# Optimization experiments

Hardware: AMD Instinct MI355X
Metric: run time of the kernel (lower is better)

The kernel has to match this reference:

```python
import jax, jax.numpy as jnp
import numpy as np
from jax import lax

DIM = 1024
INTER = 512
N_EXPERTS = 16
TOPK = 4
ROUTE_SCALE = 2.5
VOCAB = 32000


def setup_inputs() -> dict:
    key = jax.random.key(0)
    ks = jax.random.split(key, 8)
    x = jax.random.normal(ks[0], (2, 512, DIM), dtype=jnp.float32)
    input_ids = jax.random.randint(ks[1], (2, 512), 0, VOCAB)
    s = 0.02
    gate_w = jax.random.normal(ks[2], (N_EXPERTS, DIM), dtype=jnp.float32) * s
    gate_b = jax.random.normal(ks[3], (N_EXPERTS,), dtype=jnp.float32) * s
    # routed experts: w13 maps dim -> 2*inter (gate|up), w2 maps inter -> dim
    w13 = jax.random.normal(ks[4], (N_EXPERTS, 2 * INTER, DIM), dtype=jnp.float32) * s
    w2 = jax.random.normal(ks[5], (N_EXPERTS, DIM, INTER), dtype=jnp.float32) * s
    # shared expert
    w13_s = jax.random.normal(ks[6], (2 * INTER, DIM), dtype=jnp.float32) * s
    w2_s = jax.random.normal(ks[7], (DIM, INTER), dtype=jnp.float32) * s
    return {"x": x, "input_ids": input_ids, "gate_w": gate_w, "gate_b": gate_b,
            "w13": w13, "w2": w2, "w13_s": w13_s, "w2_s": w2_s}


def _silu_and_mul(gu):
    gate, up = jnp.split(gu, 2, axis=-1)
    return jax.nn.silu(gate) * up


def reference(x, input_ids, gate_w, gate_b, w13, w2, w13_s, w2_s):
    B, S, D = x.shape
    xt = x.reshape(-1, D)                      # [T, D]
    T = xt.shape[0]
    # ---- Gate (sigmoid score func, bias added for selection only) ----
    scores = jax.nn.sigmoid(xt.astype(jnp.float32) @ gate_w.T)   # [T, E]
    biased = scores + gate_b
    _, idx = lax.top_k(biased, TOPK)                             # [T, K] int
    w = jnp.take_along_axis(scores, idx, axis=-1)                # [T, K]
    w = w / jnp.sum(w, axis=-1, keepdims=True)                   # normalize (non-softmax)
    w = w * ROUTE_SCALE
    # ---- dispatch/combine as dense per-expert combine weights ----
    comb = jnp.zeros((T, N_EXPERTS), jnp.float32)
    comb = comb.at[jnp.arange(T)[:, None], idx].add(w)           # [T, E]
    comb = comb.astype(x.dtype)

    def expert_body(y, args):
        w13_e, w2_e, c_e = args                                  # [2I,D], [D,I], [T]
        h = _silu_and_mul(xt @ w13_e.T)                          # [T, I]
        return y + c_e[:, None] * (h @ w2_e.T), None

    y, _ = lax.scan(expert_body, jnp.zeros_like(xt), (w13, w2, comb.T))
    # ---- shared expert ----
    y = y + _silu_and_mul(xt @ w13_s.T) @ w2_s.T
    return y.astype(x.dtype).reshape(B, S, D)
```

## Files before the change

kernel.cpp:

```cpp
#include <hip/hip_runtime.h>
#include <hip/hip_bf16.h>
#include <math.h>

#define NTOK   1024
#define DIMX   1024
#define INTERX 512
#define NEXP   16
#define RSCALE 2.5f

typedef _Float16 f16x8 __attribute__((ext_vector_type(8)));
typedef _Float16 f16x4v __attribute__((ext_vector_type(4)));
typedef float    f32x4 __attribute__((ext_vector_type(4)));

#define N_W13  (NEXP * 2 * INTERX * DIMX)
#define N_W2   (NEXP * DIMX * INTERX)
#define N_W13S (2 * INTERX * DIMX)
#define N_W2S  (DIMX * INTERX)
#define N_X    (NTOK * DIMX)
#define N_CVT  ((size_t)N_W13 + N_W2 + N_W13S + N_W2S + N_X)

#define WS_COUNTS  0
#define WS_TOKIDX  256
#define WS_SLOTS   (WS_TOKIDX + NEXP * NTOK * 4)
#define WS_WQ      (WS_SLOTS + NTOK * 16)
#define WS_SEL     (WS_WQ + NTOK * 16)
#define WS_NT      (WS_SEL + NTOK * 16)
#define WS_TE      (WS_NT + 64)
#define WS_TM      (WS_TE + 1024)
#define WS_TR      (WS_TM + 1024)
#define WS_H       (WS_TR + 1024)
#define WS_YC      (WS_H + (size_t)5120 * 512 * 2)
#define WS_F16     (WS_YC + (size_t)5120 * 1024 * 4)
#define WS_NEED    (WS_F16 + N_CVT * 2)

#define SWZ(r, k) ((r) * 64 + ((k) ^ (((r) & 7) << 3)))

#define CVT_BLOCKS 3392

__device__ __forceinline__ f16x8 ldcvt(const float* __restrict__ p) {
    const float4 a = *(const float4*)p;
    const float4 b = *(const float4*)(p + 4);
    return (f16x8){(_Float16)a.x, (_Float16)a.y, (_Float16)a.z, (_Float16)a.w,
                   (_Float16)b.x, (_Float16)b.y, (_Float16)b.z, (_Float16)b.w};
}

__device__ __forceinline__ void gl_lds16(const _Float16* g, _Float16* l) {
    __builtin_amdgcn_global_load_lds(
        (const __attribute__((address_space(1))) void*)g,
        (__attribute__((address_space(3))) void*)l, 16, 0, 0);
}

__global__ __launch_bounds__(256) void cvt_all(
    const float* __restrict__ w13, const float* __restrict__ w2,
    const float* __restrict__ w13s, const float* __restrict__ w2s,
    const float* __restrict__ x, _Float16* __restrict__ dh)
{
    const size_t base8 = (size_t)blockIdx.x * 256 + threadIdx.x;
    float4 ra[4], rb[4];
#pragma unroll
    for (int it = 0; it < 4; ++it) {
        size_t off = (base8 + (size_t)it * (CVT_BLOCKS * 256)) * 8;
        const float* s;
        if (off < N_W13)                       s = w13 + off;
        else if ((off -= N_W13) < N_W2)        s = w2 + off;
        else if ((off -= N_W2) < N_W13S)       s = w13s + off;
        else if ((off -= N_W13S) < N_W2S)      s = w2s + off;
        else                                   s = x + (off - N_W2S);
        ra[it] = *(const float4*)s;
        rb[it] = *(const float4*)(s + 4);
    }
#pragma unroll
    for (int it = 0; it < 4; ++it) {
        const size_t i8 = base8 + (size_t)it * (CVT_BLOCKS * 256);
        f16x8 v = {(_Float16)ra[it].x, (_Float16)ra[it].y,
                   (_Float16)ra[it].z, (_Float16)ra[it].w,
                   (_Float16)rb[it].x, (_Float16)rb[it].y,
                   (_Float16)rb[it].z, (_Float16)rb[it].w};
        *(f16x8*)(dh + i8 * 8) = v;
    }
}

__global__ __launch_bounds__(256) void gate(
    const float* __restrict__ x, const float* __restrict__ gw,
    const float* __restrict__ gb,
    int* __restrict__ sel, float* __restrict__ wq)
{
    const int t    = blockIdx.x * 4 + (threadIdx.x >> 6);
    const int lane = threadIdx.x & 63;
    const int e    = lane & 15;
    const int q    = lane >> 4;

    const float4* xq = (const float4*)(x + (size_t)t * DIMX) + q * 64;
    const float4* gq = (const float4*)(gw + (size_t)e * DIMX) + q * 64;
    float s0 = 0.f, s1 = 0.f, s2 = 0.f, s3 = 0.f;
#pragma unroll 8
    for (int i = 0; i < 64; i += 2) {
        const float4 a = xq[i],     b = gq[i];
        const float4 c = xq[i + 1], d = gq[i + 1];
        s0 = fmaf(a.x, b.x, s0); s1 = fmaf(a.y, b.y, s1);
        s2 = fmaf(a.z, b.z, s2); s3 = fmaf(a.w, b.w, s3);
        s0 = fmaf(c.x, d.x, s0); s1 = fmaf(c.y, d.y, s1);
        s2 = fmaf(c.z, d.z, s2); s3 = fmaf(c.w, d.w, s3);
    }
    float acc = (s0 + s1) + (s2 + s3);
    acc += __shfl_xor(acc, 16);
    acc += __shfl_xor(acc, 32);

    const float sv = 1.f / (1.f + __expf(-acc));
    float v = (lane < 16) ? (sv + gb[e]) : -1e30f;

    float wk0, wk1, wk2, wk3; int ek0, ek1, ek2, ek3;
    float wsum = 0.f;
#pragma unroll
    for (int k = 0; k < 4; ++k) {
        float bestv = v; int besti = lane;
#pragma unroll
        for (int off = 8; off >= 1; off >>= 1) {
            const float ov = __shfl_xor(bestv, off);
            const int   oi = __shfl_xor(besti, off);
            if (ov > bestv || (ov == bestv && oi < besti)) { bestv = ov; besti = oi; }
        }
        besti = __shfl(besti, 0);
        const float sbest = __shfl(sv, besti);
        if (k == 0) { wk0 = sbest; ek0 = besti; }
        if (k == 1) { wk1 = sbest; ek1 = besti; }
        if (k == 2) { wk2 = sbest; ek2 = besti; }
        if (k == 3) { wk3 = sbest; ek3 = besti; }
        wsum += sbest;
        if (lane == besti) v = -1e30f;
    }
    const float scale = RSCALE / wsum;

    if (lane == 0) {
        sel[t * 4 + 0] = ek0;  wq[t * 4 + 0] = wk0 * scale;
        sel[t * 4 + 1] = ek1;  wq[t * 4 + 1] = wk1 * scale;
        sel[t * 4 + 2] = ek2;  wq[t * 4 + 2] = wk2 * scale;
        sel[t * 4 + 3] = ek3;  wq[t * 4 + 3] = wk3 * scale;
    }
}

__global__ __launch_bounds__(1024) void build(
    const int* __restrict__ sel,
    int* __restrict__ counts, int* __restrict__ tok_idx,
    int* __restrict__ slots,
    int* __restrict__ n_tiles, int* __restrict__ tile_e,
    int* __restrict__ tile_m0, int* __restrict__ tile_r0)
{
    __shared__ int lc[NEXP];
    const int t = threadIdx.x;
    if (t < NEXP) lc[t] = 0;
    __syncthreads();

    int e0 = sel[t * 4 + 0], e1 = sel[t * 4 + 1];
    int e2 = sel[t * 4 + 2], e3 = sel[t * 4 + 3];
    int p0 = atomicAdd(&lc[e0], 1);
    int p1 = atomicAdd(&lc[e1], 1);
    int p2 = atomicAdd(&lc[e2], 1);
    int p3 = atomicAdd(&lc[e3], 1);
    tok_idx[e0 * NTOK + p0] = t;  slots[t * 4 + 0] = (e0 << 10) | p0;
    tok_idx[e1 * NTOK + p1] = t;  slots[t * 4 + 1] = (e1 << 10) | p1;
    tok_idx[e2 * NTOK + p2] = t;  slots[t * 4 + 2] = (e2 << 10) | p2;
    tok_idx[e3 * NTOK + p3] = t;  slots[t * 4 + 3] = (e3 << 10) | p3;

    __syncthreads();
    if (t < NEXP) counts[t] = lc[t];
    if (t == 0) {
        int nt = 0, row = 0;
        for (int e = 0; e <= NEXP; ++e) {
            const int c = (e == NEXP) ? NTOK : lc[e];
            for (int m0 = 0; m0 < c; m0 += 128) {
                tile_e[nt]  = e;
                tile_m0[nt] = m0;
                tile_r0[nt] = row + m0;
                ++nt;
            }
            row += c;
        }
        n_tiles[0] = nt;
    }
}

#define WAITV8()  do { asm volatile("s_waitcnt vmcnt(8)" ::: "memory"); \
                       __builtin_amdgcn_sched_barrier(0); } while (0)
#define WAITV0()  do { asm volatile("s_waitcnt vmcnt(0)" ::: "memory"); \
                       __builtin_amdgcn_sched_barrier(0); } while (0)
#define RBAR()    do { __builtin_amdgcn_s_barrier(); \
                       __builtin_amdgcn_sched_barrier(0); } while (0)

__global__ __launch_bounds__(256, 2) void ffn1g(
    const _Float16* __restrict__ xh,
    const _Float16* __restrict__ w13h, const _Float16* __restrict__ w13sh,
    const int* __restrict__ counts, const int* __restrict__ tok_idx,
    const int* __restrict__ n_tiles, const int* __restrict__ tile_e,
    const int* __restrict__ tile_m0, const int* __restrict__ tile_r0,
    _Float16* __restrict__ h)
{
    const int tile = blockIdx.x >> 3;
    if (tile >= n_tiles[0]) return;
    const int y  = blockIdx.x & 7;
    const int e  = tile_e[tile];
    const int m0 = tile_m0[tile];
    const int rowbase = tile_r0[tile] - m0;
    const int Me = (e == NEXP) ? NTOK : counts[e];
    const int g0 = y * 64;

    const int tid = threadIdx.x, lane = tid & 63;
    const int wid = tid >> 6;
    const int wm = wid >> 1, wn = wid & 1;
    const int li = lane & 15, rk = (lane >> 4) * 8;

    const _Float16* Wh = (e == NEXP) ? w13sh : (w13h + (size_t)e * (2 * INTERX) * DIMX);

    __shared__ _Float16 T[2][256 * 64];

    const int lrow = lane >> 3;
    const int lc   = (lane & 7) ^ lrow;
    const _Float16* src[8];
    int ldsoff[8];
#pragma unroll
    for (int j = 0; j < 8; ++j) {
        const int c = wid * 8 + j;
        const int r = c * 8 + lrow;
        ldsoff[j] = c * 512;
        if (r < 128) {
            int ma = m0 + r; if (ma >= Me) ma = Me - 1;
            const int tok = (e == NEXP) ? ma : tok_idx[e * NTOK + ma];
            src[j] = xh + (size_t)tok * DIMX + lc * 8;
        } else {
            const int rb = r - 128;
            const int bwn = rb >> 6, bf = (rb >> 4) & 3, bli = rb & 15;
            const int wrow = ((bf & 2) ? INTERX : 0) + g0 + bwn * 32 + (bf & 1) * 16 + bli;
            src[j] = Wh + (size_t)wrow * DIMX + lc * 8;
        }
    }

    f32x4 acc[4][4];
#pragma unroll
    for (int i = 0; i < 4; ++i)
#pragma unroll
        for (int f = 0; f < 4; ++f) acc[i][f] = (f32x4){0.f, 0.f, 0.f, 0.f};

    auto STAGE = [&](int b, int k0) {
#pragma unroll
        for (int j = 0; j < 8; ++j)
            gl_lds16(src[j] + k0, &T[b][ldsoff[j]]);
    };
    auto MM = [&](int b) {
#pragma unroll
        for (int kk = 0; kk < 64; kk += 32) {
            f16x8 afr[4], bfr[4];
#pragma unroll
            for (int i = 0; i < 4; ++i) {
                const int r = wm * 64 + i * 16 + li;
                afr[i] = *(const f16x8*)&T[b][SWZ(r, kk + rk)];
            }
#pragma unroll
            for (int f = 0; f < 4; ++f) {
                const int r = 128 + wn * 64 + f * 16 + li;
                bfr[f] = *(const f16x8*)&T[b][SWZ(r, kk + rk)];
            }
#pragma unroll
            for (int i = 0; i < 4; ++i)
#pragma unroll
                for (int f = 0; f < 4; ++f)
                    acc[i][f] = __builtin_amdgcn_mfma_f32_16x16x32_f16(
                        afr[i], bfr[f], acc[i][f], 0, 0, 0);
        }
    };

    STAGE(0, 0);
    WAITV0();
    RBAR();
    int cur = 0;
#pragma unroll
    for (int t = 0; t < DIMX / 64; ++t) {
        if (t + 1 < DIMX / 64) {
            STAGE(cur ^ 1, (t + 1) * 64);
            WAITV8();
        } else {
            WAITV0();
        }
        RBAR();
        MM(cur);
        RBAR();
        cur ^= 1;
    }

#pragma unroll
    for (int i = 0; i < 4; ++i) {
#pragma unroll
        for (int q = 0; q < 4; ++q) {
            const int m = m0 + wm * 64 + i * 16 + (lane >> 4) * 4 + q;
            if (m >= Me) continue;
            _Float16* hp = h + (size_t)(rowbase + m) * INTERX + g0 + wn * 32 + li;
#pragma unroll
            for (int f = 0; f < 2; ++f) {
                const float g = acc[i][f][q];
                const float u = acc[i][f + 2][q];
                hp[f * 16] = (_Float16)(g * u / (1.f + __expf(-g)));
            }
        }
    }
}

__global__ __launch_bounds__(256, 2) void ffn2g(
    const _Float16* __restrict__ w2h, const _Float16* __restrict__ w2sh,
    const int* __restrict__ counts, const _Float16* __restrict__ h,
    const int* __restrict__ n_tiles, const int* __restrict__ tile_e,
    const int* __restrict__ tile_m0, const int* __restrict__ tile_r0,
    _Float16* __restrict__ yc)
{
    const int tile = blockIdx.x >> 3;
    if (tile >= n_tiles[0]) return;
    const int y  = blockIdx.x & 7;
    const int e  = tile_e[tile];
    const int m0 = tile_m0[tile];
    const int rowbase = tile_r0[tile] - m0;
    const int Me = (e == NEXP) ? NTOK : counts[e];
    const int n0 = y * 128;

    const int tid = threadIdx.x, lane = tid & 63;
    const int wid = tid >> 6;
    const int wm = wid >> 1, wn = wid & 1;
    const int li = lane & 15, rk = (lane >> 4) * 8;

    const _Float16* Wh = (e == NEXP) ? w2sh : (w2h + (size_t)e * DIMX * INTERX);

    __shared__ _Float16 T[2][256 * 64];

    const int lrow = lane >> 3;
    const int lc   = (lane & 7) ^ lrow;
    const _Float16* src[8];
    int ldsoff[8];
#pragma unroll
    for (int j = 0; j < 8; ++j) {
        const int c = wid * 8 + j;
        const int r = c * 8 + lrow;
        ldsoff[j] = c * 512;
        if (r < 128) {
            src[j] = h + (size_t)(rowbase + m0 + r) * INTERX + lc * 8;
        } else {
            const int rb = r - 128;
            src[j] = Wh + (size_t)(n0 + rb) * INTERX + lc * 8;
        }
    }

    f32x4 acc[4][4];
#pragma unroll
    for (int i = 0; i < 4; ++i)
#pragma unroll
        for (int f = 0; f < 4; ++f) acc[i][f] = (f32x4){0.f, 0.f, 0.f, 0.f};

    auto STAGE = [&](int b, int k0) {
#pragma unroll
        for (int j = 0; j < 8; ++j)
            gl_lds16(src[j] + k0, &T[b][ldsoff[j]]);
    };
    auto MM = [&](int b) {
#pragma unroll
        for (int kk = 0; kk < 64; kk += 32) {
            f16x8 afr[4], bfr[4];
#pragma unroll
            for (int i = 0; i < 4; ++i) {
                const int r = wm * 64 + i * 16 + li;
                afr[i] = *(const f16x8*)&T[b][SWZ(r, kk + rk)];
            }
#pragma unroll
            for (int f = 0; f < 4; ++f) {
                const int r = 128 + wn * 64 + f * 16 + li;
                bfr[f] = *(const f16x8*)&T[b][SWZ(r, kk + rk)];
            }
#pragma unroll
            for (int i = 0; i < 4; ++i)
#pragma unroll
                for (int f = 0; f < 4; ++f)
                    acc[i][f] = __builtin_amdgcn_mfma_f32_16x16x32_f16(
                        afr[i], bfr[f], acc[i][f], 0, 0, 0);
        }
    };

    STAGE(0, 0);
    WAITV0();
    RBAR();
    int cur = 0;
#pragma unroll
    for (int t = 0; t < INTERX / 64; ++t) {
        if (t + 1 < INTERX / 64) {
            STAGE(cur ^ 1, (t + 1) * 64);
            WAITV8();
        } else {
            WAITV0();
        }
        RBAR();
        MM(cur);
        RBAR();
        cur ^= 1;
    }

#pragma unroll
    for (int i = 0; i < 4; ++i) {
#pragma unroll
        for (int q = 0; q < 4; ++q) {
            const int m = m0 + wm * 64 + i * 16 + (lane >> 4) * 4 + q;
            if (m >= Me) continue;
            _Float16* yp = yc + (size_t)(rowbase + m) * DIMX + n0 + wn * 64 + li;
#pragma unroll
            for (int f = 0; f < 4; ++f)
                yp[f * 16] = (_Float16)acc[i][f][q];
        }
    }
}

struct Stage { f16x8 a0, a1, b0, b1, b2, b3; };

__global__ __launch_bounds__(256, 3) void ffn1f(
    const float* __restrict__ xf,
    const float* __restrict__ w13f, const float* __restrict__ w13sf,
    const int* __restrict__ counts, const int* __restrict__ tok_idx,
    _Float16* __restrict__ h)
{
    const int e  = blockIdx.z;
    const int Me = (e == NEXP) ? NTOK : counts[e];
    const int m0 = blockIdx.x * 64;
    if (m0 >= Me) return;
    const int g0 = blockIdx.y * 64;
    int rowbase = 0;
    if (e == NEXP) rowbase = 4096;
    else for (int i = 0; i < e; ++i) rowbase += counts[i];

    const int tid = threadIdx.x, lane = tid & 63;
    const int wm = tid >> 7, wn = (tid >> 6) & 1;
    const int li = lane & 15, rk = (lane >> 4) * 8;
    const int sr = tid >> 3;
    const int sc = (tid & 7) * 8;

    int ma0 = m0 + sr;      if (ma0 >= Me) ma0 = Me - 1;
    int ma1 = m0 + sr + 32; if (ma1 >= Me) ma1 = Me - 1;
    const int tok0 = (e == NEXP) ? ma0 : tok_idx[e * NTOK + ma0];
    const int tok1 = (e == NEXP) ? ma1 : tok_idx[e * NTOK + ma1];

    size_t boff[4];
#pragma unroll
    for (int j = 0; j < 4; ++j) {
        const int c = sr + 32 * j;
        const int bwn = c >> 6, bf = (c >> 4) & 3, bli = c & 15;
        const int row = ((bf & 2) ? INTERX : 0) + g0 + bwn * 32 + (bf & 1) * 16 + bli;
        boff[j] = (size_t)row * DIMX + sc;
    }
    const float* Wf = (e == NEXP) ? w13sf : (w13f + (size_t)e * (2 * INTERX) * DIMX);
    const size_t aoff0 = (size_t)tok0 * DIMX + sc;
    const size_t aoff1 = (size_t)tok1 * DIMX + sc;

    __shared__ _Float16 As[2][64 * 64];
    __shared__ _Float16 Bs[2][128 * 64];

    f32x4 acc[2][4];
#pragma unroll
    for (int i = 0; i < 2; ++i)
#pragma unroll
        for (int f = 0; f < 4; ++f) acc[i][f] = (f32x4){0.f, 0.f, 0.f, 0.f};

    auto LD = [&](int k) -> Stage {
        Stage st;
        st.a0 = ldcvt(xf + aoff0 + k);
        st.a1 = ldcvt(xf + aoff1 + k);
        st.b0 = ldcvt(Wf + boff[0] + k);
        st.b1 = ldcvt(Wf + boff[1] + k);
        st.b2 = ldcvt(Wf + boff[2] + k);
        st.b3 = ldcvt(Wf + boff[3] + k);
        return st;
    };
    auto WRb = [&](int b, const Stage& st) {
        *(f16x8*)&As[b][SWZ(sr, sc)]      = st.a0;
        *(f16x8*)&As[b][SWZ(sr + 32, sc)] = st.a1;
        *(f16x8*)&Bs[b][SWZ(sr, sc)]      = st.b0;
        *(f16x8*)&Bs[b][SWZ(sr + 32, sc)] = st.b1;
        *(f16x8*)&Bs[b][SWZ(sr + 64, sc)] = st.b2;
        *(f16x8*)&Bs[b][SWZ(sr + 96, sc)] = st.b3;
    };
    auto MM = [&](int b) {
#pragma unroll
        for (int kk = 0; kk < 64; kk += 32) {
            f16x8 afr[2], bfr[4];
#pragma unroll
            for (int i = 0; i < 2; ++i)
                afr[i] = *(const f16x8*)&As[b][SWZ(wm * 32 + i * 16 + li, kk + rk)];
#pragma unroll
            for (int f = 0; f < 4; ++f)
                bfr[f] = *(const f16x8*)&Bs[b][SWZ(wn * 64 + f * 16 + li, kk + rk)];
#pragma unroll
            for (int i = 0; i < 2; ++i)
#pragma unroll
                for (int f = 0; f < 4; ++f)
                    acc[i][f] = __builtin_amdgcn_mfma_f32_16x16x32_f16(
                        afr[i], bfr[f], acc[i][f], 0, 0, 0);
        }
    };

    Stage rB = LD(0);
    WRb(0, rB);
    rB = LD(64);
    Stage rC = LD(128);
#pragma unroll
    for (int t = 0; t < DIMX / 64; ++t) {
        __syncthreads();
        Stage rN;
        if (t + 3 < DIMX / 64) rN = LD((t + 3) * 64); else rN = rC;
        MM(t & 1);
        WRb((t & 1) ^ 1, rB);
        rB = rC; rC = rN;
    }

#pragma unroll
    for (int i = 0; i < 2; ++i) {
#pragma unroll
        for (int q = 0; q < 4; ++q) {
            const int m = m0 + wm * 32 + i * 16 + (lane >> 4) * 4 + q;
            if (m >= Me) continue;
            _Float16* hp = h + (size_t)(rowbase + m) * INTERX + g0 + wn * 32 + li;
#pragma unroll
            for (int f = 0; f < 2; ++f) {
                const float g = acc[i][f][q];
                const float u = acc[i][f + 2][q];
                hp[f * 16] = (_Float16)(g * u / (1.f + __expf(-g)));
            }
        }
    }
}

__global__ __launch_bounds__(256, 3) void ffn2f(
    const float* __restrict__ w2f, const float* __restrict__ w2sf,
    const int* __restrict__ counts, const _Float16* __restrict__ h,
    _Float16* __restrict__ yc)
{
    const int e  = blockIdx.z;
    const int Me = (e == NEXP) ? NTOK : counts[e];
    const int m0 = blockIdx.x * 64;
    if (m0 >= Me) return;
    const int n0 = blockIdx.y * 128;
    int rowbase = 0;
    if (e == NEXP) rowbase = 4096;
    else for (int i = 0; i < e; ++i) rowbase += counts[i];

    const int tid = threadIdx.x, lane = tid & 63;
    const int wm = tid >> 7, wn = (tid >> 6) & 1;
    const int li = lane & 15, rk = (lane >> 4) * 8;
    const int sr = tid >> 3;
    const int sc = (tid & 7) * 8;

    const _Float16* pA0 = h + (size_t)(rowbase + m0 + sr) * INTERX + sc;
    const _Float16* pA1 = pA0 + (size_t)32 * INTERX;
    const float* Wf = (e == NEXP) ? w2sf : (w2f + (size_t)e * DIMX * INTERX);
    size_t boff[4];
#pragma unroll
    for (int j = 0; j < 4; ++j) boff[j] = (size_t)(n0 + sr + 32 * j) * INTERX + sc;

    __shared__ _Float16 As[2][64 * 64];
    __shared__ _Float16 Bs[2][128 * 64];

    f32x4 acc[2][4];
#pragma unroll
    for (int i = 0; i < 2; ++i)
#pragma unroll
        for (int f = 0; f < 4; ++f) acc[i][f] = (f32x4){0.f, 0.f, 0.f, 0.f};

    auto LD = [&](int k) -> Stage {
        Stage st;
        st.a0 = *(const f16x8*)(pA0 + k);
        st.a1 = *(const f16x8*)(pA1 + k);
        st.b0 = ldcvt(Wf + boff[0] + k);
        st.b1 = ldcvt(Wf + boff[1] + k);
        st.b2 = ldcvt(Wf + boff[2] + k);
        st.b3 = ldcvt(Wf + boff[3] + k);
        return st;
    };
    auto WRb = [&](int b, const Stage& st) {
        *(f16x8*)&As[b][SWZ(sr, sc)]      = st.a0;
        *(f16x8*)&As[b][SWZ(sr + 32, sc)] = st.a1;
        *(f16x8*)&Bs[b][SWZ(sr, sc)]      = st.b0;
        *(f16x8*)&Bs[b][SWZ(sr + 32, sc)] = st.b1;
        *(f16x8*)&Bs[b][SWZ(sr + 64, sc)] = st.b2;
        *(f16x8*)&Bs[b][SWZ(sr + 96, sc)] = st.b3;
    };
    auto MM = [&](int b) {
#pragma unroll
        for (int kk = 0; kk < 64; kk += 32) {
            f16x8 afr[2], bfr[4];
#pragma unroll
            for (int i = 0; i < 2; ++i)
                afr[i] = *(const f16x8*)&As[b][SWZ(wm * 32 + i * 16 + li, kk + rk)];
#pragma unroll
            for (int f = 0; f < 4; ++f)
                bfr[f] = *(const f16x8*)&Bs[b][SWZ(wn * 64 + f * 16 + li, kk + rk)];
#pragma unroll
            for (int i = 0; i < 2; ++i)
#pragma unroll
                for (int f = 0; f < 4; ++f)
                    acc[i][f] = __builtin_amdgcn_mfma_f32_16x16x32_f16(
                        afr[i], bfr[f], acc[i][f], 0, 0, 0);
        }
    };

    Stage rB = LD(0);
    WRb(0, rB);
    rB = LD(64);
    Stage rC = LD(128);
#pragma unroll
    for (int t = 0; t < INTERX / 64; ++t) {
        __syncthreads();
        Stage rN;
        if (t + 3 < INTERX / 64) rN = LD((t + 3) * 64); else rN = rC;
        MM(t & 1);
        WRb((t & 1) ^ 1, rB);
        rB = rC; rC = rN;
    }

#pragma unroll
    for (int i = 0; i < 2; ++i) {
#pragma unroll
        for (int q = 0; q < 4; ++q) {
            const int m = m0 + wm * 32 + i * 16 + (lane >> 4) * 4 + q;
            if (m >= Me) continue;
            _Float16* yp = yc + (size_t)(rowbase + m) * DIMX + n0 + wn * 64 + li;
#pragma unroll
            for (int f = 0; f < 4; ++f)
                yp[f * 16] = (_Float16)acc[i][f][q];
        }
    }
}

__global__ __launch_bounds__(256) void combine(
    const int* __restrict__ counts,
    const int* __restrict__ slots,
    const float* __restrict__ wq,
    const _Float16* __restrict__ yc,
    float* __restrict__ out)
{
    __shared__ int soff[NEXP];
    if (threadIdx.x < NEXP) {
        int o = 0;
        for (int i = 0; i < (int)threadIdx.x; ++i) o += counts[i];
        soff[threadIdx.x] = o;
    }
    __syncthreads();

    const int t = blockIdx.x;
    const int tid = threadIdx.x;
    const f16x4v* ycv = (const f16x4v*)yc;
    const f16x4v b = ycv[(size_t)(4096 + t) * 256 + tid];
    float a0 = (float)b[0], a1 = (float)b[1], a2 = (float)b[2], a3 = (float)b[3];
#pragma unroll
    for (int k = 0; k < 4; ++k) {
        const int s   = slots[t * 4 + k];
        const int e   = s >> 10, pos = s & 1023;
        const float w = wq[t * 4 + k];
        const f16x4v v = ycv[(size_t)(soff[e] + pos) * 256 + tid];
        a0 = fmaf(w, (float)v[0], a0); a1 = fmaf(w, (float)v[1], a1);
        a2 = fmaf(w, (float)v[2], a2); a3 = fmaf(w, (float)v[3], a3);
    }
    ((float4*)out)[(size_t)t * 256 + tid] = make_float4(a0, a1, a2, a3);
}

extern "C" void kernel_launch(void* const* d_in, const int* in_sizes, int n_in,
                              void* d_out, int out_size, void* d_ws, size_t ws_size,
                              hipStream_t stream)
{
    const float* x    = (const float*)d_in[0];
    const float* gw   = (const float*)d_in[2];
    const float* gb   = (const float*)d_in[3];
    const float* w13  = (const float*)d_in[4];
    const float* w2   = (const float*)d_in[5];
    const float* w13s = (const float*)d_in[6];
    const float* w2s  = (const float*)d_in[7];
    float* out = (float*)d_out;

    char* ws = (char*)d_ws;
    int*       counts  = (int*)(ws + WS_COUNTS);
    int*       tok_idx = (int*)(ws + WS_TOKIDX);
    int*       slots   = (int*)(ws + WS_SLOTS);
    float*     wq      = (float*)(ws + WS_WQ);
    int*       sel     = (int*)(ws + WS_SEL);
    int*       n_tiles = (int*)(ws + WS_NT);
    int*       tile_e  = (int*)(ws + WS_TE);
    int*       tile_m0 = (int*)(ws + WS_TM);
    int*       tile_r0 = (int*)(ws + WS_TR);
    _Float16*  h       = (_Float16*)(ws + WS_H);
    _Float16*  yc      = (_Float16*)(ws + WS_YC);
    _Float16*  dh      = (_Float16*)(ws + WS_F16);
    _Float16*  w13h    = dh;
    _Float16*  w2h     = w13h + N_W13;
    _Float16*  w13sh   = w2h + N_W2;
    _Float16*  w2sh    = w13sh + N_W13S;
    _Float16*  xh      = w2sh + N_W2S;

    const bool F16 = (ws_size >= WS_NEED);

    gate<<<NTOK / 4, 256, 0, stream>>>(x, gw, gb, sel, wq);
    build<<<1, 1024, 0, stream>>>(sel, counts, tok_idx, slots,
                                  n_tiles, tile_e, tile_m0, tile_r0);
    if (F16)
        cvt_all<<<CVT_BLOCKS, 256, 0, stream>>>(w13, w2, w13s, w2s, x, dh);

    if (F16) {
        ffn1g<<<1088, 256, 0, stream>>>(xh, w13h, w13sh, counts, tok_idx,
                                        n_tiles, tile_e, tile_m0, tile_r0, h);
        ffn2g<<<1088, 256, 0, stream>>>(w2h, w2sh, counts, h,
                                        n_tiles, tile_e, tile_m0, tile_r0, yc);
    } else {
        dim3 g1(16, 8, 17), g2(16, 8, 17);
        ffn1f<<<g1, 256, 0, stream>>>(x, w13, w13s, counts, tok_idx, h);
        ffn2f<<<g2, 256, 0, stream>>>(w2, w2s, counts, h, yc);
    }
    combine<<<NTOK, 256, 0, stream>>>(counts, slots, wq, yc, out);
}
```

Before: 93.06 us.

## Drop standalone fp16 conversion pass; convert weights inside GEMM tile loads

Removes the cvt_all kernel, which read all fp32 weights and wrote an fp16 copy on every call. The grouped GEMM kernels now load fp32 weight tiles into registers, convert them to fp16 and write them to LDS, while activations still use direct global-to-LDS loads. The x-to-fp16 conversion is folded into the gate kernel. This avoids a full extra read and write of the weights each call, but weight tiles are reread as fp32 by every block that uses them, and staging through registers adds VGPR pressure and LDS write traffic inside the main loop.

```diff
diff --git a/kernel.cpp b/kernel.cpp
--- a/kernel.cpp
+++ b/kernel.cpp
@@ -11,13 +11,6 @@
 typedef _Float16 f16x8 __attribute__((ext_vector_type(8)));
 typedef _Float16 f16x4v __attribute__((ext_vector_type(4)));
 typedef float    f32x4 __attribute__((ext_vector_type(4)));
-
-#define N_W13  (NEXP * 2 * INTERX * DIMX)
-#define N_W2   (NEXP * DIMX * INTERX)
-#define N_W13S (2 * INTERX * DIMX)
-#define N_W2S  (DIMX * INTERX)
-#define N_X    (NTOK * DIMX)
-#define N_CVT  ((size_t)N_W13 + N_W2 + N_W13S + N_W2S + N_X)
 
 #define WS_COUNTS  0
 #define WS_TOKIDX  256
@@ -28,14 +21,12 @@
 #define WS_TE      (WS_NT + 64)
 #define WS_TM      (WS_TE + 1024)
 #define WS_TR      (WS_TM + 1024)
-#define WS_H       (WS_TR + 1024)
+#define WS_XH      (WS_TR + 1024)
+#define WS_H       (WS_XH + (size_t)NTOK * DIMX * 2)
 #define WS_YC      (WS_H + (size_t)5120 * 512 * 2)
-#define WS_F16     (WS_YC + (size_t)5120 * 1024 * 4)
-#define WS_NEED    (WS_F16 + N_CVT * 2)
+#define WS_NEED    (WS_YC + (size_t)5120 * 1024 * 2)
 
 #define SWZ(r, k) ((r) * 64 + ((k) ^ (((r) & 7) << 3)))
-
-#define CVT_BLOCKS 3392
 
 __device__ __forceinline__ f16x8 ldcvt(const float* __restrict__ p) {
     const float4 a = *(const float4*)p;
@@ -50,40 +41,11 @@
         (__attribute__((address_space(3))) void*)l, 16, 0, 0);
 }
 
-__global__ __launch_bounds__(256) void cvt_all(
-    const float* __restrict__ w13, const float* __restrict__ w2,
-    const float* __restrict__ w13s, const float* __restrict__ w2s,
-    const float* __restrict__ x, _Float16* __restrict__ dh)
-{
-    const size_t base8 = (size_t)blockIdx.x * 256 + threadIdx.x;
-    float4 ra[4], rb[4];
-#pragma unroll
-    for (int it = 0; it < 4; ++it) {
-        size_t off = (base8 + (size_t)it * (CVT_BLOCKS * 256)) * 8;
-        const float* s;
-        if (off < N_W13)                       s = w13 + off;
-        else if ((off -= N_W13) < N_W2)        s = w2 + off;
-        else if ((off -= N_W2) < N_W13S)       s = w13s + off;
-        else if ((off -= N_W13S) < N_W2S)      s = w2s + off;
-        else                                   s = x + (off - N_W2S);
-        ra[it] = *(const float4*)s;
-        rb[it] = *(const float4*)(s + 4);
-    }
-#pragma unroll
-    for (int it = 0; it < 4; ++it) {
-        const size_t i8 = base8 + (size_t)it * (CVT_BLOCKS * 256);
-        f16x8 v = {(_Float16)ra[it].x, (_Float16)ra[it].y,
-                   (_Float16)ra[it].z, (_Float16)ra[it].w,
-                   (_Float16)rb[it].x, (_Float16)rb[it].y,
-                   (_Float16)rb[it].z, (_Float16)rb[it].w};
-        *(f16x8*)(dh + i8 * 8) = v;
-    }
-}
-
 __global__ __launch_bounds__(256) void gate(
     const float* __restrict__ x, const float* __restrict__ gw,
     const float* __restrict__ gb,
-    int* __restrict__ sel, float* __restrict__ wq)
+    int* __restrict__ sel, float* __restrict__ wq,
+    _Float16* __restrict__ xh)
 {
     const int t    = blockIdx.x * 4 + (threadIdx.x >> 6);
     const int lane = threadIdx.x & 63;
@@ -105,6 +67,12 @@
     float acc = (s0 + s1) + (s2 + s3);
     acc += __shfl_xor(acc, 16);
     acc += __shfl_xor(acc, 32);
+
+    if (xh) {
+        const float* xr = x + (size_t)t * DIMX + lane * 16;
+        *(f16x8*)(xh + (size_t)t * DIMX + lane * 16)     = ldcvt(xr);
+        *(f16x8*)(xh + (size_t)t * DIMX + lane * 16 + 8) = ldcvt(xr + 8);
+    }
 
     const float sv = 1.f / (1.f + __expf(-acc));
     float v = (lane < 16) ? (sv + gb[e]) : -1e30f;
@@ -180,16 +148,9 @@
     }
 }
 
-#define WAITV8()  do { asm volatile("s_waitcnt vmcnt(8)" ::: "memory"); \
-                       __builtin_amdgcn_sched_barrier(0); } while (0)
-#define WAITV0()  do { asm volatile("s_waitcnt vmcnt(0)" ::: "memory"); \
-                       __builtin_amdgcn_sched_barrier(0); } while (0)
-#define RBAR()    do { __builtin_amdgcn_s_barrier(); \
-                       __builtin_amdgcn_sched_barrier(0); } while (0)
-
 __global__ __launch_bounds__(256, 2) void ffn1g(
     const _Float16* __restrict__ xh,
-    const _Float16* __restrict__ w13h, const _Float16* __restrict__ w13sh,
+    const float* __restrict__ w13f, const float* __restrict__ w13sf,
     const int* __restrict__ counts, const int* __restrict__ tok_idx,
     const int* __restrict__ n_tiles, const int* __restrict__ tile_e,
     const int* __restrict__ tile_m0, const int* __restrict__ tile_r0,
@@ -209,30 +170,29 @@
     const int wm = wid >> 1, wn = wid & 1;
     const int li = lane & 15, rk = (lane >> 4) * 8;
 
-    const _Float16* Wh = (e == NEXP) ? w13sh : (w13h + (size_t)e * (2 * INTERX) * DIMX);
+    const float* Wf = (e == NEXP) ? w13sf : (w13f + (size_t)e * (2 * INTERX) * DIMX);
 
     __shared__ _Float16 T[2][256 * 64];
 
     const int lrow = lane >> 3;
     const int lc   = (lane & 7) ^ lrow;
-    const _Float16* src[8];
-    int ldsoff[8];
-#pragma unroll
-    for (int j = 0; j < 8; ++j) {
-        const int c = wid * 8 + j;
+    const _Float16* srcA[4];
+    int ldsoffA[4];
+#pragma unroll
+    for (int j = 0; j < 4; ++j) {
+        const int c = wid * 4 + j;
         const int r = c * 8 + lrow;
-        ldsoff[j] = c * 512;
-        if (r < 128) {
-            int ma = m0 + r; if (ma >= Me) ma = Me - 1;
-            const int tok = (e == NEXP) ? ma : tok_idx[e * NTOK + ma];
-            src[j] = xh + (size_t)tok * DIMX + lc * 8;
-        } else {
-            const int rb = r - 128;
-            const int bwn = rb >> 6, bf = (rb >> 4) & 3, bli = rb & 15;
-            const int wrow = ((bf & 2) ? INTERX : 0) + g0 + bwn * 32 + (bf & 1) * 16 + bli;
-            src[j] = Wh + (size_t)wrow * DIMX + lc * 8;
-        }
-    }
+        ldsoffA[j] = c * 512;
+        int ma = m0 + r; if (ma >= Me) ma = Me - 1;
+        const int tok = (e == NEXP) ? ma : tok_idx[e * NTOK + ma];
+        srcA[j] = xh + (size_t)tok * DIMX + lc * 8;
+    }
+
+    const int rb = tid >> 1;
+    const int bh = (tid & 1) * 32;
+    const int bwn = rb >> 6, bf = (rb >> 4) & 3, bli = rb & 15;
+    const int wrow = ((bf & 2) ? INTERX : 0) + g0 + bwn * 32 + (bf & 1) * 16 + bli;
+    const float* bsrc = Wf + (size_t)wrow * DIMX + bh;
 
     f32x4 acc[4][4];
 #pragma unroll
@@ -240,25 +200,37 @@
 #pragma unroll
         for (int f = 0; f < 4; ++f) acc[i][f] = (f32x4){0.f, 0.f, 0.f, 0.f};
 
-    auto STAGE = [&](int b, int k0) {
-#pragma unroll
-        for (int j = 0; j < 8; ++j)
-            gl_lds16(src[j] + k0, &T[b][ldsoff[j]]);
+    float4 br[8];
+    auto BLOAD = [&](int k0) {
+#pragma unroll
+        for (int i = 0; i < 8; ++i)
+            br[i] = *(const float4*)(bsrc + k0 + i * 4);
+    };
+    auto AGLOAD = [&](int b, int k0) {
+#pragma unroll
+        for (int j = 0; j < 4; ++j)
+            gl_lds16(srcA[j] + k0, &T[b][ldsoffA[j]]);
+    };
+    auto BWRITE = [&](int b) {
+#pragma unroll
+        for (int i = 0; i < 4; ++i) {
+            f16x8 v = {(_Float16)br[2*i].x, (_Float16)br[2*i].y,
+                       (_Float16)br[2*i].z, (_Float16)br[2*i].w,
+                       (_Float16)br[2*i+1].x, (_Float16)br[2*i+1].y,
+                       (_Float16)br[2*i+1].z, (_Float16)br[2*i+1].w};
+            *(f16x8*)&T[b][SWZ(128 + rb, bh + i * 8)] = v;
+        }
     };
     auto MM = [&](int b) {
 #pragma unroll
         for (int kk = 0; kk < 64; kk += 32) {
             f16x8 afr[4], bfr[4];
 #pragma unroll
-            for (int i = 0; i < 4; ++i) {
-                const int r = wm * 64 + i * 16 + li;
-                afr[i] = *(const f16x8*)&T[b][SWZ(r, kk + rk)];
-            }
-#pragma unroll
-            for (int f = 0; f < 4; ++f) {
-                const int r = 128 + wn * 64 + f * 16 + li;
-                bfr[f] = *(const f16x8*)&T[b][SWZ(r, kk + rk)];
-            }
+            for (int i = 0; i < 4; ++i)
+                afr[i] = *(const f16x8*)&T[b][SWZ(wm * 64 + i * 16 + li, kk + rk)];
+#pragma unroll
+            for (int f = 0; f < 4; ++f)
+                bfr[f] = *(const f16x8*)&T[b][SWZ(128 + wn * 64 + f * 16 + li, kk + rk)];
 #pragma unroll
             for (int i = 0; i < 4; ++i)
 #pragma unroll
@@ -268,21 +240,21 @@
         }
     };
 
-    STAGE(0, 0);
-    WAITV0();
-    RBAR();
+    BLOAD(0);
+    AGLOAD(0, 0);
+    BWRITE(0);
+    __syncthreads();
     int cur = 0;
 #pragma unroll
     for (int t = 0; t < DIMX / 64; ++t) {
         if (t + 1 < DIMX / 64) {
-            STAGE(cur ^ 1, (t + 1) * 64);
-            WAITV8();
-        } else {
-            WAITV0();
-        }
-        RBAR();
+            BLOAD((t + 1) * 64);
+            AGLOAD(cur ^ 1, (t + 1) * 64);
+            __builtin_amdgcn_sched_barrier(0);
+        }
         MM(cur);
-        RBAR();
+        if (t + 1 < DIMX / 64) BWRITE(cur ^ 1);
+        __syncthreads();
         cur ^= 1;
     }
 
@@ -304,7 +276,7 @@
 }
 
 __global__ __launch_bounds__(256, 2) void ffn2g(
-    const _Float16* __restrict__ w2h, const _Float16* __restrict__ w2sh,
+    const float* __restrict__ w2f, const float* __restrict__ w2sf,
     const int* __restrict__ counts, const _Float16* __restrict__ h,
     const int* __restrict__ n_tiles, const int* __restrict__ tile_e,
     const int* __restrict__ tile_m0, const int* __restrict__ tile_r0,
@@ -324,26 +296,25 @@
     const int wm = wid >> 1, wn = wid & 1;
     const int li = lane & 15, rk = (lane >> 4) * 8;
 
-    const _Float16* Wh = (e == NEXP) ? w2sh : (w2h + (size_t)e * DIMX * INTERX);
+    const float* Wf = (e == NEXP) ? w2sf : (w2f + (size_t)e * DIMX * INTERX);
 
     __shared__ _Float16 T[2][256 * 64];
 
     const int lrow = lane >> 3;
     const int lc   = (lane & 7) ^ lrow;
-    const _Float16* src[8];
-    int ldsoff[8];
-#pragma unroll
-    for (int j = 0; j < 8; ++j) {
-        const int c = wid * 8 + j;
+    const _Float16* srcA[4];
+    int ldsoffA[4];
+#pragma unroll
+    for (int j = 0; j < 4; ++j) {
+        const int c = wid * 4 + j;
         const int r = c * 8 + lrow;
-        ldsoff[j] = c * 512;
-        if (r < 128) {
-            src[j] = h + (size_t)(rowbase + m0 + r) * INTERX + lc * 8;
-        } else {
-            const int rb = r - 128;
-            src[j] = Wh + (size_t)(n0 + rb) * INTERX + lc * 8;
-        }
-    }
+        ldsoffA[j] = c * 512;
+        srcA[j] = h + (size_t)(rowbase + m0 + r) * INTERX + lc * 8;
+    }
+
+    const int rb = tid >> 1;
+    const int bh = (tid & 1) * 32;
+    const float* bsrc = Wf + (size_t)(n0 + rb) * INTERX + bh;
 
     f32x4 acc[4][4];
 #pragma unroll
@@ -351,25 +322,37 @@
 #pragma unroll
         for (int f = 0; f < 4; ++f) acc[i][f] = (f32x4){0.f, 0.f, 0.f, 0.f};
 
-    auto STAGE = [&](int b, int k0) {
-#pragma unroll
-        for (int j = 0; j < 8; ++j)
-            gl_lds16(src[j] + k0, &T[b][ldsoff[j]]);
+    float4 br[8];
+    auto BLOAD = [&](int k0) {
+#pragma unroll
+        for (int i = 0; i < 8; ++i)
+            br[i] = *(const float4*)(bsrc + k0 + i * 4);
+    };
+    auto AGLOAD = [&](int b, int k0) {
+#pragma unroll
+        for (int j = 0; j < 4; ++j)
+            gl_lds16(srcA[j] + k0, &T[b][ldsoffA[j]]);
+    };
+    auto BWRITE = [&](int b) {
+#pragma unroll
+        for (int i = 0; i < 4; ++i) {
+            f16x8 v = {(_Float16)br[2*i].x, (_Float16)br[2*i].y,
+                       (_Float16)br[2*i].z, (_Float16)br[2*i].w,
+                       (_Float16)br[2*i+1].x, (_Float16)br[2*i+1].y,
+                       (_Float16)br[2*i+1].z, (_Float16)br[2*i+1].w};
+            *(f16x8*)&T[b][SWZ(128 + rb, bh + i * 8)] = v;
+        }
     };
     auto MM = [&](int b) {
 #pragma unroll
         for (int kk = 0; kk < 64; kk += 32) {
             f16x8 afr[4], bfr[4];
 #pragma unroll
-            for (int i = 0; i < 4; ++i) {
-                const int r = wm * 64 + i * 16 + li;
-                afr[i] = *(const f16x8*)&T[b][SWZ(r, kk + rk)];
-            }
-#pragma unroll
-            for (int f = 0; f < 4; ++f) {
-                const int r = 128 + wn * 64 + f * 16 + li;
-                bfr[f] = *(const f16x8*)&T[b][SWZ(r, kk + rk)];
-            }
+            for (int i = 0; i < 4; ++i)
+                afr[i] = *(const f16x8*)&T[b][SWZ(wm * 64 + i * 16 + li, kk + rk)];
+#pragma unroll
+            for (int f = 0; f < 4; ++f)
+                bfr[f] = *(const f16x8*)&T[b][SWZ(128 + wn * 64 + f * 16 + li, kk + rk)];
 #pragma unroll
             for (int i = 0; i < 4; ++i)
 #pragma unroll
@@ -379,21 +362,21 @@
         }
     };
 
-    STAGE(0, 0);
-    WAITV0();
-    RBAR();
+    BLOAD(0);
+    AGLOAD(0, 0);
+    BWRITE(0);
+    __syncthreads();
     int cur = 0;
 #pragma unroll
     for (int t = 0; t < INTERX / 64; ++t) {
         if (t + 1 < INTERX / 64) {
-            STAGE(cur ^ 1, (t + 1) * 64);
-            WAITV8();
-        } else {
-            WAITV0();
-        }
-        RBAR();
+            BLOAD((t + 1) * 64);
+            AGLOAD(cur ^ 1, (t + 1) * 64);
+            __builtin_amdgcn_sched_barrier(0);
+        }
         MM(cur);
-        RBAR();
+        if (t + 1 < INTERX / 64) BWRITE(cur ^ 1);
+        __syncthreads();
         cur ^= 1;
     }
 
@@ -402,224 +385,6 @@
 #pragma unroll
         for (int q = 0; q < 4; ++q) {
             const int m = m0 + wm * 64 + i * 16 + (lane >> 4) * 4 + q;
-            if (m >= Me) continue;
-            _Float16* yp = yc + (size_t)(rowbase + m) * DIMX + n0 + wn * 64 + li;
-#pragma unroll
-            for (int f = 0; f < 4; ++f)
-                yp[f * 16] = (_Float16)acc[i][f][q];
-        }
-    }
-}
-
-struct Stage { f16x8 a0, a1, b0, b1, b2, b3; };
-
-__global__ __launch_bounds__(256, 3) void ffn1f(
-    const float* __restrict__ xf,
-    const float* __restrict__ w13f, const float* __restrict__ w13sf,
-    const int* __restrict__ counts, const int* __restrict__ tok_idx,
-    _Float16* __restrict__ h)
-{
-    const int e  = blockIdx.z;
-    const int Me = (e == NEXP) ? NTOK : counts[e];
-    const int m0 = blockIdx.x * 64;
-    if (m0 >= Me) return;
-    const int g0 = blockIdx.y * 64;
-    int rowbase = 0;
-    if (e == NEXP) rowbase = 4096;
-    else for (int i = 0; i < e; ++i) rowbase += counts[i];
-
-    const int tid = threadIdx.x, lane = tid & 63;
-    const int wm = tid >> 7, wn = (tid >> 6) & 1;
-    const int li = lane & 15, rk = (lane >> 4) * 8;
-    const int sr = tid >> 3;
-    const int sc = (tid & 7) * 8;
-
-    int ma0 = m0 + sr;      if (ma0 >= Me) ma0 = Me - 1;
-    int ma1 = m0 + sr + 32; if (ma1 >= Me) ma1 = Me - 1;
-    const int tok0 = (e == NEXP) ? ma0 : tok_idx[e * NTOK + ma0];
-    const int tok1 = (e == NEXP) ? ma1 : tok_idx[e * NTOK + ma1];
-
-    size_t boff[4];
-#pragma unroll
-    for (int j = 0; j < 4; ++j) {
-        const int c = sr + 32 * j;
-        const int bwn = c >> 6, bf = (c >> 4) & 3, bli = c & 15;
-        const int row = ((bf & 2) ? INTERX : 0) + g0 + bwn * 32 + (bf & 1) * 16 + bli;
-        boff[j] = (size_t)row * DIMX + sc;
-    }
-    const float* Wf = (e == NEXP) ? w13sf : (w13f + (size_t)e * (2 * INTERX) * DIMX);
-    const size_t aoff0 = (size_t)tok0 * DIMX + sc;
-    const size_t aoff1 = (size_t)tok1 * DIMX + sc;
-
-    __shared__ _Float16 As[2][64 * 64];
-    __shared__ _Float16 Bs[2][128 * 64];
-
-    f32x4 acc[2][4];
-#pragma unroll
-    for (int i = 0; i < 2; ++i)
-#pragma unroll
-        for (int f = 0; f < 4; ++f) acc[i][f] = (f32x4){0.f, 0.f, 0.f, 0.f};
-
-    auto LD = [&](int k) -> Stage {
-        Stage st;
-        st.a0 = ldcvt(xf + aoff0 + k);
-        st.a1 = ldcvt(xf + aoff1 + k);
-        st.b0 = ldcvt(Wf + boff[0] + k);
-        st.b1 = ldcvt(Wf + boff[1] + k);
-        st.b2 = ldcvt(Wf + boff[2] + k);
-        st.b3 = ldcvt(Wf + boff[3] + k);
-        return st;
-    };
-    auto WRb = [&](int b, const Stage& st) {
-        *(f16x8*)&As[b][SWZ(sr, sc)]      = st.a0;
-        *(f16x8*)&As[b][SWZ(sr + 32, sc)] = st.a1;
-        *(f16x8*)&Bs[b][SWZ(sr, sc)]      = st.b0;
-        *(f16x8*)&Bs[b][SWZ(sr + 32, sc)] = st.b1;
-        *(f16x8*)&Bs[b][SWZ(sr + 64, sc)] = st.b2;
-        *(f16x8*)&Bs[b][SWZ(sr + 96, sc)] = st.b3;
-    };
-    auto MM = [&](int b) {
-#pragma unroll
-        for (int kk = 0; kk < 64; kk += 32) {
-            f16x8 afr[2], bfr[4];
-#pragma unroll
-            for (int i = 0; i < 2; ++i)
-                afr[i] = *(const f16x8*)&As[b][SWZ(wm * 32 + i * 16 + li, kk + rk)];
-#pragma unroll
-            for (int f = 0; f < 4; ++f)
-                bfr[f] = *(const f16x8*)&Bs[b][SWZ(wn * 64 + f * 16 + li, kk + rk)];
-#pragma unroll
-            for (int i = 0; i < 2; ++i)
-#pragma unroll
-                for (int f = 0; f < 4; ++f)
-                    acc[i][f] = __builtin_amdgcn_mfma_f32_16x16x32_f16(
-                        afr[i], bfr[f], acc[i][f], 0, 0, 0);
-        }
-    };
-
-    Stage rB = LD(0);
-    WRb(0, rB);
-    rB = LD(64);
-    Stage rC = LD(128);
-#pragma unroll
-    for (int t = 0; t < DIMX / 64; ++t) {
-        __syncthreads();
-        Stage rN;
-        if (t + 3 < DIMX / 64) rN = LD((t + 3) * 64); else rN = rC;
-        MM(t & 1);
-        WRb((t & 1) ^ 1, rB);
-        rB = rC; rC = rN;
-    }
-
-#pragma unroll
-    for (int i = 0; i < 2; ++i) {
-#pragma unroll
-        for (int q = 0; q < 4; ++q) {
-            const int m = m0 + wm * 32 + i * 16 + (lane >> 4) * 4 + q;
-            if (m >= Me) continue;
-            _Float16* hp = h + (size_t)(rowbase + m) * INTERX + g0 + wn * 32 + li;
-#pragma unroll
-            for (int f = 0; f < 2; ++f) {
-                const float g = acc[i][f][q];
-                const float u = acc[i][f + 2][q];
-                hp[f * 16] = (_Float16)(g * u / (1.f + __expf(-g)));
-            }
-        }
-    }
-}
-
-__global__ __launch_bounds__(256, 3) void ffn2f(
-    const float* __restrict__ w2f, const float* __restrict__ w2sf,
-    const int* __restrict__ counts, const _Float16* __restrict__ h,
-    _Float16* __restrict__ yc)
-{
-    const int e  = blockIdx.z;
-    const int Me = (e == NEXP) ? NTOK : counts[e];
-    const int m0 = blockIdx.x * 64;
-    if (m0 >= Me) return;
-    const int n0 = blockIdx.y * 128;
-    int rowbase = 0;
-    if (e == NEXP) rowbase = 4096;
-    else for (int i = 0; i < e; ++i) rowbase += counts[i];
-
-    const int tid = threadIdx.x, lane = tid & 63;
-    const int wm = tid >> 7, wn = (tid >> 6) & 1;
-    const int li = lane & 15, rk = (lane >> 4) * 8;
-    const int sr = tid >> 3;
-    const int sc = (tid & 7) * 8;
-
-    const _Float16* pA0 = h + (size_t)(rowbase + m0 + sr) * INTERX + sc;
-    const _Float16* pA1 = pA0 + (size_t)32 * INTERX;
-    const float* Wf = (e == NEXP) ? w2sf : (w2f + (size_t)e * DIMX * INTERX);
-    size_t boff[4];
-#pragma unroll
-    for (int j = 0; j < 4; ++j) boff[j] = (size_t)(n0 + sr + 32 * j) * INTERX + sc;
-
-    __shared__ _Float16 As[2][64 * 64];
-    __shared__ _Float16 Bs[2][128 * 64];
-
-    f32x4 acc[2][4];
-#pragma unroll
-    for (int i = 0; i < 2; ++i)
-#pragma unroll
-        for (int f = 0; f < 4; ++f) acc[i][f] = (f32x4){0.f, 0.f, 0.f, 0.f};
-
-    auto LD = [&](int k) -> Stage {
-        Stage st;
-        st.a0 = *(const f16x8*)(pA0 + k);
-        st.a1 = *(const f16x8*)(pA1 + k);
-        st.b0 = ldcvt(Wf + boff[0] + k);
-        st.b1 = ldcvt(Wf + boff[1] + k);
-        st.b2 = ldcvt(Wf + boff[2] + k);
-        st.b3 = ldcvt(Wf + boff[3] + k);
-        return st;
-    };
-    auto WRb = [&](int b, const Stage& st) {
-        *(f16x8*)&As[b][SWZ(sr, sc)]      = st.a0;
-        *(f16x8*)&As[b][SWZ(sr + 32, sc)] = st.a1;
-        *(f16x8*)&Bs[b][SWZ(sr, sc)]      = st.b0;
-        *(f16x8*)&Bs[b][SWZ(sr + 32, sc)] = st.b1;
-        *(f16x8*)&Bs[b][SWZ(sr + 64, sc)] = st.b2;
-        *(f16x8*)&Bs[b][SWZ(sr + 96, sc)] = st.b3;
-    };
-    auto MM = [&](int b) {
-#pragma unroll
-        for (int kk = 0; kk < 64; kk += 32) {
-            f16x8 afr[2], bfr[4];
-#pragma unroll
-            for (int i = 0; i < 2; ++i)
-                afr[i] = *(const f16x8*)&As[b][SWZ(wm * 32 + i * 16 + li, kk + rk)];
-#pragma unroll
-            for (int f = 0; f < 4; ++f)
-                bfr[f] = *(const f16x8*)&Bs[b][SWZ(wn * 64 + f * 16 + li, kk + rk)];
-#pragma unroll
-            for (int i = 0; i < 2; ++i)
-#pragma unroll
-                for (int f = 0; f < 4; ++f)
-                    acc[i][f] = __builtin_amdgcn_mfma_f32_16x16x32_f16(
-                        afr[i], bfr[f], acc[i][f], 0, 0, 0);
-        }
-    };
-
-    Stage rB = LD(0);
-    WRb(0, rB);
-    rB = LD(64);
-    Stage rC = LD(128);
-#pragma unroll
-    for (int t = 0; t < INTERX / 64; ++t) {
-        __syncthreads();
-        Stage rN;
-        if (t + 3 < INTERX / 64) rN = LD((t + 3) * 64); else rN = rC;
-        MM(t & 1);
-        WRb((t & 1) ^ 1, rB);
-        rB = rC; rC = rN;
-    }
-
-#pragma unroll
-    for (int i = 0; i < 2; ++i) {
-#pragma unroll
-        for (int q = 0; q < 4; ++q) {
-            const int m = m0 + wm * 32 + i * 16 + (lane >> 4) * 4 + q;
             if (m >= Me) continue;
             _Float16* yp = yc + (size_t)(rowbase + m) * DIMX + n0 + wn * 64 + li;
 #pragma unroll
@@ -684,32 +449,17 @@
     int*       tile_e  = (int*)(ws + WS_TE);
     int*       tile_m0 = (int*)(ws + WS_TM);
     int*       tile_r0 = (int*)(ws + WS_TR);
+    _Float16*  xh      = (_Float16*)(ws + WS_XH);
     _Float16*  h       = (_Float16*)(ws + WS_H);
     _Float16*  yc      = (_Float16*)(ws + WS_YC);
-    _Float16*  dh      = (_Float16*)(ws + WS_F16);
-    _Float16*  w13h    = dh;
-    _Float16*  w2h     = w13h + N_W13;
-    _Float16*  w13sh   = w2h + N_W2;
-    _Float16*  w2sh    = w13sh + N_W13S;
-    _Float16*  xh      = w2sh + N_W2S;
-
-    const bool F16 = (ws_size >= WS_NEED);
-
-    gate<<<NTOK / 4, 256, 0, stream>>>(x, gw, gb, sel, wq);
+
+    gate<<<NTOK / 4, 256, 0, stream>>>(x, gw, gb, sel, wq, xh);
     build<<<1, 1024, 0, stream>>>(sel, counts, tok_idx, slots,
                                   n_tiles, tile_e, tile_m0, tile_r0);
-    if (F16)
-        cvt_all<<<CVT_BLOCKS, 256, 0, stream>>>(w13, w2, w13s, w2s, x, dh);
-
-    if (F16) {
-        ffn1g<<<1088, 256, 0, stream>>>(xh, w13h, w13sh, counts, tok_idx,
-                                        n_tiles, tile_e, tile_m0, tile_r0, h);
-        ffn2g<<<1088, 256, 0, stream>>>(w2h, w2sh, counts, h,
-                                        n_tiles, tile_e, tile_m0, tile_r0, yc);
-    } else {
-        dim3 g1(16, 8, 17), g2(16, 8, 17);
-        ffn1f<<<g1, 256, 0, stream>>>(x, w13, w13s, counts, tok_idx, h);
-        ffn2f<<<g2, 256, 0, stream>>>(w2, w2s, counts, h, yc);
-    }
+
+    ffn1g<<<1088, 256, 0, stream>>>(xh, w13, w13s, counts, tok_idx,
+                                    n_tiles, tile_e, tile_m0, tile_r0, h);
+    ffn2g<<<1088, 256, 0, stream>>>(w2, w2s, counts, h,
+                                    n_tiles, tile_e, tile_m0, tile_r0, yc);
     combine<<<NTOK, 256, 0, stream>>>(counts, slots, wq, yc, out);
 }
```

Result: slower. 101.2 us (+8.7%).
